# Performance work log

Hardware: AMD Instinct MI355X
Metric: run time of the kernel (lower is better)

## Reference

```python
import jax, jax.numpy as jnp
import numpy as np

MARGIN = 0.3


def setup_inputs() -> dict:
    key = jax.random.key(0)
    k1, k2 = jax.random.split(key)
    inputs = jax.random.normal(k1, (8192, 128), dtype=jnp.float32)
    targets = jax.random.randint(k2, (8192,), 0, 512, dtype=jnp.int64)
    return {"inputs": inputs, "targets": targets}


def reference(inputs, targets):
    # inputs: [n, d], targets: [n]
    sq = jnp.sum(inputs * inputs, axis=1)  # [n]
    # dist[i,j] = ||x_i||^2 + ||x_j||^2 - 2 x_i . x_j
    dist = sq[:, None] + sq[None, :] - 2.0 * (inputs @ inputs.T)
    dist = jnp.sqrt(jnp.clip(dist, 1e-12, None))  # [n, n]
    mask = targets[:, None] == targets[None, :]  # True where same label
    # batch-hard mining: hardest positive (max) and hardest negative (min) per row.
    # Diagonal is always True, so every row has at least one positive.
    dist_ap = jnp.max(jnp.where(mask, dist, -jnp.inf), axis=1)  # [n]
    dist_an = jnp.min(jnp.where(mask, jnp.inf, dist), axis=1)  # [n]
    # MarginRankingLoss with y=1: mean(max(0, margin - (dist_an - dist_ap)))
    loss = jnp.mean(jnp.maximum(0.0, MARGIN - (dist_an - dist_ap)))
    prec = jnp.mean((dist_an > dist_ap).astype(jnp.float32))
    return loss, prec
```

## Files before the change

kernel.cpp:

```cpp
#include <hip/hip_runtime.h>
#include <hip/hip_bf16.h>
#include <math.h>

#define N 8192
#define D 128
#define MARGIN 0.3f

#define NSTRIP 64
#define CPS 12
#define GRID_MAIN (NSTRIP * CPS)

typedef float f32x4 __attribute__((ext_vector_type(4)));
typedef short bf16x8 __attribute__((ext_vector_type(8)));
typedef unsigned short u16x8 __attribute__((ext_vector_type(8)));

#define AS1 __attribute__((address_space(1)))
#define AS3 __attribute__((address_space(3)))

__device__ inline void gload_lds16(const void* g, void* l) {
    __builtin_amdgcn_global_load_lds((AS1 void*)(void*)(g), (AS3 void*)(l), 16, 0, 0);
}

__device__ inline unsigned short f2bf(float f) {
    unsigned u = __float_as_uint(f);
    unsigned r = (u + 0x7FFFu + ((u >> 16) & 1u)) >> 16;
    return (unsigned short)r;
}

__global__ __launch_bounds__(256) void convert_kernel(const float* __restrict__ X,
                                                      unsigned short* __restrict__ Xb,
                                                      float* __restrict__ sq,
                                                      unsigned* __restrict__ ap2,
                                                      unsigned* __restrict__ an2) {
    int tid = threadIdx.x;
    int row = blockIdx.x * 16 + (tid >> 4);
    int l = tid & 15;
    const float4* p = reinterpret_cast<const float4*>(X + (size_t)row * D + l * 8);
    float4 u = p[0];
    float4 v = p[1];
    float s = u.x*u.x + u.y*u.y + u.z*u.z + u.w*u.w
            + v.x*v.x + v.y*v.y + v.z*v.z + v.w*v.w;
    u16x8 o;
    o[0] = f2bf(u.x); o[1] = f2bf(u.y); o[2] = f2bf(u.z); o[3] = f2bf(u.w);
    o[4] = f2bf(v.x); o[5] = f2bf(v.y); o[6] = f2bf(v.z); o[7] = f2bf(v.w);
    *reinterpret_cast<u16x8*>(Xb + (size_t)row * D + l * 8) = o;
    #pragma unroll
    for (int off = 8; off >= 1; off >>= 1) s += __shfl_xor(s, off);
    if (l == 0) {
        sq[row] = s;
        ap2[row] = 0u;
        an2[row] = 0x7F7F7F7Fu;
    }
}

__global__ __launch_bounds__(256, 3) void triplet_main(
        const unsigned short* __restrict__ Xb,
        const int* __restrict__ lbl,
        const float* __restrict__ sq,
        unsigned* __restrict__ ap2,
        unsigned* __restrict__ an2) {
    __shared__ unsigned short Bs[2][64 * D];
    unsigned short* BsL = &Bs[0][0];

    const int bi = blockIdx.x / CPS;
    const int c  = blockIdx.x - bi * CPS;
    const int jt0 = c * 10 + (c < 8 ? c : 8);
    const int cnt = 10 + (c < 8 ? 1 : 0);
    const int i0 = bi * 128;

    const int tid = threadIdx.x;
    const int w = tid >> 6;
    const int lane = tid & 63;
    const int wr = w >> 1;
    const int wc = w & 1;
    const int quad = lane >> 4;
    const int lx = lane & 15;

    #pragma unroll
    for (int t = 0; t < 8; ++t) {
        int rbase = w * 32 + t * 4;
        int r = rbase + quad;
        int gc = lx ^ (r & 7);
        gload_lds16(Xb + (size_t)(i0 + r) * D + gc * 8, BsL + rbase * D);
    }

    int lbl_i[16];
    #pragma unroll
    for (int tr = 0; tr < 4; ++tr)
        #pragma unroll
        for (int v = 0; v < 4; ++v)
            lbl_i[tr * 4 + v] = lbl[i0 + wr * 64 + tr * 16 + quad * 4 + v];

    __syncthreads();

    bf16x8 af_r[4][4];
    #pragma unroll
    for (int tr = 0; tr < 4; ++tr) {
        int rA = wr * 64 + tr * 16 + lx;
        #pragma unroll
        for (int ks = 0; ks < 4; ++ks) {
            int sc = (ks * 4 + quad) ^ (lx & 7);
            af_r[tr][ks] = *reinterpret_cast<const bf16x8*>(&BsL[rA * D + sc * 8]);
        }
    }
    __syncthreads();

    {
        int jj0 = jt0;
        #pragma unroll
        for (int t = 0; t < 4; ++t) {
            int rbase = w * 16 + t * 4;
            int r = rbase + quad;
            int gc = lx ^ (r & 7);
            gload_lds16(Xb + (size_t)(jj0 * 64 + r) * D + gc * 8, BsL + rbase * D);
        }
    }

    float m_ap[16], m_an[16];
    #pragma unroll
    for (int q = 0; q < 16; ++q) { m_ap[q] = -INFINITY; m_an[q] = INFINITY; }

    __syncthreads();

    for (int tt = 0; tt < cnt; ++tt) {
        const int jj = jt0 + tt;
        const int cur = tt & 1;
        const unsigned short* curB = BsL + cur * (64 * D);

        float sqj[2]; int lblj[2];
        #pragma unroll
        for (int tc = 0; tc < 2; ++tc) {
            int jc = jj * 64 + wc * 32 + tc * 16 + lx;
            sqj[tc] = sq[jc];
            lblj[tc] = lbl[jc];
        }

        if (tt + 1 < cnt) {
            unsigned short* nb = BsL + (cur ^ 1) * (64 * D);
            int jn = jj + 1;
            #pragma unroll
            for (int t = 0; t < 4; ++t) {
                int rbase = w * 16 + t * 4;
                int r = rbase + quad;
                int gc = lx ^ (r & 7);
                gload_lds16(Xb + (size_t)(jn * 64 + r) * D + gc * 8, nb + rbase * D);
            }
        }

        f32x4 acc[4][2];
        #pragma unroll
        for (int a = 0; a < 4; ++a)
            #pragma unroll
            for (int cc = 0; cc < 2; ++cc)
                acc[a][cc] = (f32x4){0.f, 0.f, 0.f, 0.f};

        #pragma unroll
        for (int ks = 0; ks < 4; ++ks) {
            bf16x8 bf[2];
            #pragma unroll
            for (int tc = 0; tc < 2; ++tc) {
                int rB = wc * 32 + tc * 16 + lx;
                int sc = (ks * 4 + quad) ^ (lx & 7);
                bf[tc] = *reinterpret_cast<const bf16x8*>(&curB[rB * D + sc * 8]);
            }
            #pragma unroll
            for (int tr = 0; tr < 4; ++tr)
                #pragma unroll
                for (int tc = 0; tc < 2; ++tc)
                    acc[tr][tc] = __builtin_amdgcn_mfma_f32_16x16x32_bf16(
                        af_r[tr][ks], bf[tc], acc[tr][tc], 0, 0, 0);
        }

        #pragma unroll
        for (int tc = 0; tc < 2; ++tc) {
            #pragma unroll
            for (int tr = 0; tr < 4; ++tr) {
                #pragma unroll
                for (int v = 0; v < 4; ++v) {
                    int q = tr * 4 + v;
                    float vi = fmaf(-2.f, acc[tr][tc][v], sqj[tc]);
                    bool same = (lblj[tc] == lbl_i[q]);
                    m_ap[q] = same ? fmaxf(m_ap[q], vi) : m_ap[q];
                    m_an[q] = same ? m_an[q] : fminf(m_an[q], vi);
                }
            }
        }

        if (tt + 1 < cnt) __syncthreads();
    }

    #pragma unroll
    for (int off = 8; off >= 1; off >>= 1) {
        #pragma unroll
        for (int q = 0; q < 16; ++q) {
            m_ap[q] = fmaxf(m_ap[q], __shfl_xor(m_ap[q], off));
            m_an[q] = fminf(m_an[q], __shfl_xor(m_an[q], off));
        }
    }
    if (lx == 0) {
        #pragma unroll
        for (int tr = 0; tr < 4; ++tr) {
            #pragma unroll
            for (int v = 0; v < 4; ++v) {
                int q = tr * 4 + v;
                int row = i0 + wr * 64 + tr * 16 + quad * 4 + v;
                float sqi = sq[row];
                float vap = fmaxf(sqi + m_ap[q], 1e-12f);
                float van = fmaxf(sqi + m_an[q], 1e-12f);
                atomicMax(&ap2[row], __float_as_uint(vap));
                atomicMin(&an2[row], __float_as_uint(van));
            }
        }
    }
}

__global__ __launch_bounds__(1024) void finalize_kernel(const unsigned* __restrict__ ap2,
                                                        const unsigned* __restrict__ an2,
                                                        float* __restrict__ out) {
    int tid = threadIdx.x;
    float ls = 0.f, ps = 0.f;
    for (int row = tid; row < N; row += 1024) {
        float ap = sqrtf(__uint_as_float(ap2[row]));
        float an = sqrtf(__uint_as_float(an2[row]));
        ls += fmaxf(0.f, MARGIN - (an - ap));
        ps += (an > ap) ? 1.f : 0.f;
    }
    #pragma unroll
    for (int off = 32; off >= 1; off >>= 1) {
        ls += __shfl_xor(ls, off);
        ps += __shfl_xor(ps, off);
    }
    __shared__ float red[2][16];
    int w = tid >> 6;
    if ((tid & 63) == 0) { red[0][w] = ls; red[1][w] = ps; }
    __syncthreads();
    if (tid == 0) {
        float L = 0.f, P = 0.f;
        #pragma unroll
        for (int i = 0; i < 16; ++i) { L += red[0][i]; P += red[1][i]; }
        out[0] = L / (float)N;
        out[1] = P / (float)N;
    }
}

extern "C" void kernel_launch(void* const* d_in, const int* in_sizes, int n_in,
                              void* d_out, int out_size, void* d_ws, size_t ws_size,
                              hipStream_t stream) {
    const float* X = (const float*)d_in[0];
    const int* lbl = (const int*)d_in[1];
    float* out = (float*)d_out;

    float* sq = (float*)d_ws;
    unsigned* ap2 = (unsigned*)d_ws + N;
    unsigned* an2 = (unsigned*)d_ws + 2 * N;
    unsigned short* Xb = (unsigned short*)((char*)d_ws + 3 * N * sizeof(unsigned));

    convert_kernel<<<N / 16, 256, 0, stream>>>(X, Xb, sq, ap2, an2);
    triplet_main<<<GRID_MAIN, 256, 0, stream>>>(Xb, lbl, sq, ap2, an2);
    finalize_kernel<<<1, 1024, 0, stream>>>(ap2, an2, out);
}
```

Baseline: 104.8 us.

## Use 512-thread blocks with 32x32 wave tiles and even column-chunk split

Doubles the block to 8 waves, each computing a 32x32 slice instead of 64x32, which halves the per-wave accumulator and A-fragment registers so more waves can be resident. The column range is split into 8 equal chunks of 16 tiles, replacing the uneven 12-way split, and the main loop gets a fixed trip count with unroll 2. Swizzled LDS offsets are precomputed once and XORed per k-step, and the first k-step MFMA takes a zero accumulator directly. The trade-off is less MFMA work per B-fragment load and per barrier, and smaller reuse per wave.

```diff
diff --git a/kernel.cpp b/kernel.cpp
--- a/kernel.cpp
+++ b/kernel.cpp
@@ -7,7 +7,8 @@
 #define MARGIN 0.3f
 
 #define NSTRIP 64
-#define CPS 12
+#define CPS 8
+#define TPC 16
 #define GRID_MAIN (NSTRIP * CPS)
 
 typedef float f32x4 __attribute__((ext_vector_type(4)));
@@ -53,7 +54,7 @@
     }
 }
 
-__global__ __launch_bounds__(256, 3) void triplet_main(
+__global__ __launch_bounds__(512, 4) void triplet_main(
         const unsigned short* __restrict__ Xb,
         const int* __restrict__ lbl,
         const float* __restrict__ sq,
@@ -62,10 +63,9 @@
     __shared__ unsigned short Bs[2][64 * D];
     unsigned short* BsL = &Bs[0][0];
 
-    const int bi = blockIdx.x / CPS;
-    const int c  = blockIdx.x - bi * CPS;
-    const int jt0 = c * 10 + (c < 8 ? c : 8);
-    const int cnt = 10 + (c < 8 ? 1 : 0);
+    const int bi = blockIdx.x >> 3;
+    const int c  = blockIdx.x & 7;
+    const int jt0 = c * TPC;
     const int i0 = bi * 128;
 
     const int tid = threadIdx.x;
@@ -77,26 +77,26 @@
     const int lx = lane & 15;
 
     #pragma unroll
-    for (int t = 0; t < 8; ++t) {
-        int rbase = w * 32 + t * 4;
+    for (int t = 0; t < 4; ++t) {
+        int rbase = w * 16 + t * 4;
         int r = rbase + quad;
         int gc = lx ^ (r & 7);
         gload_lds16(Xb + (size_t)(i0 + r) * D + gc * 8, BsL + rbase * D);
     }
 
-    int lbl_i[16];
-    #pragma unroll
-    for (int tr = 0; tr < 4; ++tr)
+    int lbl_i[8];
+    #pragma unroll
+    for (int tr = 0; tr < 2; ++tr)
         #pragma unroll
         for (int v = 0; v < 4; ++v)
-            lbl_i[tr * 4 + v] = lbl[i0 + wr * 64 + tr * 16 + quad * 4 + v];
-
-    __syncthreads();
-
-    bf16x8 af_r[4][4];
-    #pragma unroll
-    for (int tr = 0; tr < 4; ++tr) {
-        int rA = wr * 64 + tr * 16 + lx;
+            lbl_i[tr * 4 + v] = lbl[i0 + wr * 32 + tr * 16 + quad * 4 + v];
+
+    __syncthreads();
+
+    bf16x8 af_r[2][4];
+    #pragma unroll
+    for (int tr = 0; tr < 2; ++tr) {
+        int rA = wr * 32 + tr * 16 + lx;
         #pragma unroll
         for (int ks = 0; ks < 4; ++ks) {
             int sc = (ks * 4 + quad) ^ (lx & 7);
@@ -105,27 +105,33 @@
     }
     __syncthreads();
 
-    {
-        int jj0 = jt0;
-        #pragma unroll
-        for (int t = 0; t < 4; ++t) {
-            int rbase = w * 16 + t * 4;
-            int r = rbase + quad;
-            int gc = lx ^ (r & 7);
-            gload_lds16(Xb + (size_t)(jj0 * 64 + r) * D + gc * 8, BsL + rbase * D);
-        }
-    }
-
-    float m_ap[16], m_an[16];
-    #pragma unroll
-    for (int q = 0; q < 16; ++q) { m_ap[q] = -INFINITY; m_an[q] = INFINITY; }
-
-    __syncthreads();
-
-    for (int tt = 0; tt < cnt; ++tt) {
+    #pragma unroll
+    for (int t = 0; t < 2; ++t) {
+        int rbase = w * 8 + t * 4;
+        int r = rbase + quad;
+        int gc = lx ^ (r & 7);
+        gload_lds16(Xb + (size_t)(jt0 * 64 + r) * D + gc * 8, BsL + rbase * D);
+    }
+
+    unsigned vb[2];
+    #pragma unroll
+    for (int tc = 0; tc < 2; ++tc) {
+        int rB = wc * 32 + tc * 16 + lx;
+        vb[tc] = (unsigned)(rB * 256 + ((lx & 4) << 4) + ((quad ^ (lx & 3)) << 4));
+    }
+
+    float m_ap[8], m_an[8];
+    #pragma unroll
+    for (int q = 0; q < 8; ++q) { m_ap[q] = -INFINITY; m_an[q] = INFINITY; }
+    const f32x4 z4 = {0.f, 0.f, 0.f, 0.f};
+
+    __syncthreads();
+
+    #pragma unroll 2
+    for (int tt = 0; tt < TPC; ++tt) {
         const int jj = jt0 + tt;
         const int cur = tt & 1;
-        const unsigned short* curB = BsL + cur * (64 * D);
+        const char* bsb = (const char*)BsL + cur * (64 * D * 2);
 
         float sqj[2]; int lblj[2];
         #pragma unroll
@@ -135,36 +141,39 @@
             lblj[tc] = lbl[jc];
         }
 
-        if (tt + 1 < cnt) {
+        if (tt + 1 < TPC) {
             unsigned short* nb = BsL + (cur ^ 1) * (64 * D);
             int jn = jj + 1;
             #pragma unroll
-            for (int t = 0; t < 4; ++t) {
-                int rbase = w * 16 + t * 4;
+            for (int t = 0; t < 2; ++t) {
+                int rbase = w * 8 + t * 4;
                 int r = rbase + quad;
                 int gc = lx ^ (r & 7);
                 gload_lds16(Xb + (size_t)(jn * 64 + r) * D + gc * 8, nb + rbase * D);
             }
         }
 
-        f32x4 acc[4][2];
-        #pragma unroll
-        for (int a = 0; a < 4; ++a)
-            #pragma unroll
-            for (int cc = 0; cc < 2; ++cc)
-                acc[a][cc] = (f32x4){0.f, 0.f, 0.f, 0.f};
-
-        #pragma unroll
-        for (int ks = 0; ks < 4; ++ks) {
+        f32x4 acc[2][2];
+        {
+            bf16x8 bf0[2];
+            #pragma unroll
+            for (int tc = 0; tc < 2; ++tc)
+                bf0[tc] = *reinterpret_cast<const bf16x8*>(bsb + (vb[tc] ^ 0u));
+            #pragma unroll
+            for (int tr = 0; tr < 2; ++tr)
+                #pragma unroll
+                for (int tc = 0; tc < 2; ++tc)
+                    acc[tr][tc] = __builtin_amdgcn_mfma_f32_16x16x32_bf16(
+                        af_r[tr][0], bf0[tc], z4, 0, 0, 0);
+        }
+        #pragma unroll
+        for (int ks = 1; ks < 4; ++ks) {
             bf16x8 bf[2];
             #pragma unroll
-            for (int tc = 0; tc < 2; ++tc) {
-                int rB = wc * 32 + tc * 16 + lx;
-                int sc = (ks * 4 + quad) ^ (lx & 7);
-                bf[tc] = *reinterpret_cast<const bf16x8*>(&curB[rB * D + sc * 8]);
-            }
-            #pragma unroll
-            for (int tr = 0; tr < 4; ++tr)
+            for (int tc = 0; tc < 2; ++tc)
+                bf[tc] = *reinterpret_cast<const bf16x8*>(bsb + (vb[tc] ^ (unsigned)(ks << 6)));
+            #pragma unroll
+            for (int tr = 0; tr < 2; ++tr)
                 #pragma unroll
                 for (int tc = 0; tc < 2; ++tc)
                     acc[tr][tc] = __builtin_amdgcn_mfma_f32_16x16x32_bf16(
@@ -174,7 +183,7 @@
         #pragma unroll
         for (int tc = 0; tc < 2; ++tc) {
             #pragma unroll
-            for (int tr = 0; tr < 4; ++tr) {
+            for (int tr = 0; tr < 2; ++tr) {
                 #pragma unroll
                 for (int v = 0; v < 4; ++v) {
                     int q = tr * 4 + v;
@@ -186,24 +195,24 @@
             }
         }
 
-        if (tt + 1 < cnt) __syncthreads();
+        if (tt + 1 < TPC) __syncthreads();
     }
 
     #pragma unroll
     for (int off = 8; off >= 1; off >>= 1) {
         #pragma unroll
-        for (int q = 0; q < 16; ++q) {
+        for (int q = 0; q < 8; ++q) {
             m_ap[q] = fmaxf(m_ap[q], __shfl_xor(m_ap[q], off));
             m_an[q] = fminf(m_an[q], __shfl_xor(m_an[q], off));
         }
     }
     if (lx == 0) {
         #pragma unroll
-        for (int tr = 0; tr < 4; ++tr) {
+        for (int tr = 0; tr < 2; ++tr) {
             #pragma unroll
             for (int v = 0; v < 4; ++v) {
                 int q = tr * 4 + v;
-                int row = i0 + wr * 64 + tr * 16 + quad * 4 + v;
+                int row = i0 + wr * 32 + tr * 16 + quad * 4 + v;
                 float sqi = sq[row];
                 float vap = fmaxf(sqi + m_ap[q], 1e-12f);
                 float van = fmaxf(sqi + m_an[q], 1e-12f);
@@ -256,6 +265,6 @@
     unsigned short* Xb = (unsigned short*)((char*)d_ws + 3 * N * sizeof(unsigned));
 
     convert_kernel<<<N / 16, 256, 0, stream>>>(X, Xb, sq, ap2, an2);
-    triplet_main<<<GRID_MAIN, 256, 0, stream>>>(Xb, lbl, sq, ap2, an2);
+    triplet_main<<<GRID_MAIN, 512, 0, stream>>>(Xb, lbl, sq, ap2, an2);
     finalize_kernel<<<1, 1024, 0, stream>>>(ap2, an2, out);
 }
```

Measured after the change: 93.47 us. 10.8% less time.
